# Performance work log

Measured on AMD Instinct MI355X. Metric: run time of the kernel, lower is better.

## Reference

```python
import jax, jax.numpy as jnp
import numpy as np

K = 499  # kernel_size


def setup_inputs() -> dict:
    key = jax.random.key(0)
    k1, k2 = jax.random.split(key)
    B, F, T = 32, 64, 8000
    # nonnegative spectrogram input, shape (B, 1, F, T)
    x = jax.random.uniform(k1, (B, 1, F, T), dtype=jnp.float32)
    a = 0.90 + 0.099 * jax.random.uniform(k2, (F,), dtype=jnp.float32)
    w = jnp.ones((F,), dtype=jnp.float32)
    return {"x": x, "a": a, "w": w}


def _build_kernel(a, w, dtype):
    # powers[f, k] = a_f ** k, k = 0..K-2
    F = a.shape[0]
    powers = a[:, None] ** jnp.arange(K - 1, dtype=dtype)  # (F, K-1)
    C = 1.0 / powers.sum(axis=1)                            # (F,)
    neg = (-C * w)[:, None] * powers                        # (F, K-1)
    # pre-flip kernel = [1, neg_0, ..., neg_{K-2}]; flipped -> [neg_{K-2}, ..., neg_0, 1]
    kern = jnp.concatenate([neg[:, ::-1], jnp.ones((F, 1), dtype)], axis=1)  # (F, K)
    return kern[:, None, :]  # (F, 1, K) OIH, groups = F


def reference(x, a, w):
    dtype = x.dtype
    kern = _build_kernel(a.astype(dtype), w.astype(dtype), dtype)
    xs = x[:, 0]  # (B, F, T)
    # replicate (edge) pad on the left by K-1 along time
    xp = jnp.pad(xs, ((0, 0), (0, 0), (K - 1, 0)), mode="edge")
    y = jax.lax.conv_general_dilated(
        xp, kern,
        window_strides=(1,), padding="VALID",
        dimension_numbers=("NCH", "OIH", "NCH"),
        feature_group_count=xs.shape[1],
    )  # (B, F, T)
    return jnp.abs(y)[:, None]  # (B, 1, F, T)
```

## Files before the change

### kernel.cpp

```cpp
#include <hip/hip_runtime.h>
#include <math.h>


constexpr int T     = 8000;
constexpr int F     = 64;
constexpr int B     = 32;
constexpr int KM1   = 498;
constexpr int CHUNK = 512;
constexpr int CPR   = (T + CHUNK - 1) / CHUNK;

#define DPP_F(x, ctrl, rm) \
  __builtin_bit_cast(float, __builtin_amdgcn_update_dpp(0, __builtin_bit_cast(int, (x)), (ctrl), (rm), 0xf, false))

__device__ __forceinline__ double dpow(double b, int e) {
    double r = 1.0, p = b;
    while (e) { if (e & 1) r *= p; p *= p; e >>= 1; }
    return r;
}

__device__ __forceinline__ float powi(float base, int e) {
    float r = 1.0f, p = base;
    #pragma unroll
    for (int b = 0; b < 9; ++b) { r = (e & (1 << b)) ? r * p : r; p *= p; }
    return r;
}

__global__ __launch_bounds__(256) void willmore_scan_kernel(
    const float* __restrict__ x, const float* __restrict__ a,
    const float* __restrict__ w, float* __restrict__ out)
{
    const int wid   = blockIdx.x * 4 + (threadIdx.x >> 6);
    const int lane  = threadIdx.x & 63;
    const int row   = wid >> 4;
    const int chunk = wid & (CPR - 1);
    const int f     = row % F;

    const float* xr   = x   + (size_t)row * T;
    float*       orow = out + (size_t)row * T;

    const double ad     = (double)a[f];
    const double a498d  = dpow(ad, KM1);
    const double sumgeo = (1.0 - a498d) / (1.0 - ad);
    const double r_d    = dpow(ad, 8);
    const float  af     = (float)ad;
    const float  na498  = (float)(-a498d);
    const float  g      = (float)(1.0 / sumgeo) * w[f];
    const float  r1     = (float)r_d;
    const float  r2     = (float)(r_d * r_d);
    const float  r4     = (float)dpow(r_d, 4);
    const float  r8     = (float)dpow(r_d, 8);
    const float  inv_r  = (float)(1.0 / r_d);
    const float  alane  = powi(af, 8 * lane);
    const float  wA     = powi(af, 8 * ((lane & 15) + 1));
    const float  wB     = powi(af, 8 * ((lane & 31) + 1));

    const int t0   = chunk * CHUNK;
    const int tb_u = t0 + 8 * lane;
    const int tb   = min(tb_u, T - 8);

    const float4 m0 = *(const float4*)(xr + tb);
    const float4 m1 = *(const float4*)(xr + tb + 4);

    float ws8[8];
    float lv[8];
    const int lg = tb - KM1;
    if (chunk > 0) {
        const int wb = t0 - CHUNK + 8 * lane;
        const float4 w0 = *(const float4*)(xr + wb);
        const float4 w1 = *(const float4*)(xr + wb + 4);
        ws8[0]=w0.x; ws8[1]=w0.y; ws8[2]=w0.z; ws8[3]=w0.w;
        ws8[4]=w1.x; ws8[5]=w1.y; ws8[6]=w1.z; ws8[7]=w1.w;
        const float2 p0 = *(const float2*)(xr + lg);
        const float2 p1 = *(const float2*)(xr + lg + 2);
        const float2 p2 = *(const float2*)(xr + lg + 4);
        const float2 p3 = *(const float2*)(xr + lg + 6);
        lv[0]=p0.x; lv[1]=p0.y; lv[2]=p1.x; lv[3]=p1.y;
        lv[4]=p2.x; lv[5]=p2.y; lv[6]=p3.x; lv[7]=p3.y;
    } else {
        #pragma unroll
        for (int i = 0; i < 8; ++i) lv[i] = xr[max(lg + i, 0)];
    }

    float S;
    if (chunk == 0) {
        S = m0.x;
        S = xr[0] * (float)sumgeo;
    } else {
        #pragma unroll
        for (int i = 0; i < 8; ++i) { if (8 * lane + i < 14) ws8[i] = 0.0f; }
        float h = ws8[0];
        #pragma unroll
        for (int i = 1; i < 8; ++i) h = fmaf(h, af, ws8[i]);
        float contrib = powi(af, 504 - 8 * lane) * h;
        #pragma unroll
        for (int s = 1; s < 64; s <<= 1) contrib += __shfl_xor(contrib, s, 64);
        S = contrib;
    }

    const float xv[8] = {m0.x, m0.y, m0.z, m0.w, m1.x, m1.y, m1.z, m1.w};
    float u[8];
    #pragma unroll
    for (int i = 0; i < 8; ++i) u[i] = fmaf(na498, lv[i], xv[i]);

    float q = u[0];
    #pragma unroll
    for (int i = 1; i < 8; ++i) q = fmaf(q, af, u[i]);

    float G = q;
    G = fmaf(r1, DPP_F(G, 0x111, 0xf), G);
    G = fmaf(r2, DPP_F(G, 0x112, 0xf), G);
    G = fmaf(r4, DPP_F(G, 0x114, 0xf), G);
    G = fmaf(r8, DPP_F(G, 0x118, 0xf), G);
    G = fmaf(wA, DPP_F(G, 0x142, 0xa), G);
    G = fmaf(wB, DPP_F(G, 0x143, 0xc), G);

    const float E = (G - q) * inv_r;

    float s = fmaf(alane, S, E);
    float y[8];
    #pragma unroll
    for (int i = 0; i < 8; ++i) {
        y[i] = fabsf(fmaf(-g, s, xv[i]));
        s = fmaf(af, s, u[i]);
    }

    if (tb_u <= T - 8) {
        *(float4*)(orow + tb)     = make_float4(y[0], y[1], y[2], y[3]);
        *(float4*)(orow + tb + 4) = make_float4(y[4], y[5], y[6], y[7]);
    }
}

extern "C" void kernel_launch(void* const* d_in, const int* in_sizes, int n_in,
                              void* d_out, int out_size, void* d_ws, size_t ws_size,
                              hipStream_t stream) {
    const float* x = (const float*)d_in[0];
    const float* a = (const float*)d_in[1];
    const float* w = (const float*)d_in[2];
    float* out = (float*)d_out;

    const int blocks = B * F * CPR / 4;
    hipLaunchKernelGGL(willmore_scan_kernel, dim3(blocks), dim3(256), 0, stream,
                       x, a, w, out);
}
```

Baseline: 116.6 us.

## Stage each row in LDS with one 1024-thread block per row

Launches one 1024-thread block per (batch, band) row and stages the whole row in shared memory. Each wave then reads its previous-chunk window and lagged samples from LDS instead of issuing extra global loads. This removes the redundant global reads (roughly 2x traffic) of overlapping windows. The cost is a block-wide barrier, fewer resident blocks because of the large block size and 32KB of LDS, and unaligned scalar LDS reads for the lagged values.

```diff
diff --git a/kernel.cpp b/kernel.cpp
--- a/kernel.cpp
+++ b/kernel.cpp
@@ -7,7 +7,7 @@
 constexpr int B     = 32;
 constexpr int KM1   = 498;
 constexpr int CHUNK = 512;
-constexpr int CPR   = (T + CHUNK - 1) / CHUNK;
+constexpr int CPR   = 16;
 
 #define DPP_F(x, ctrl, rm) \
   __builtin_bit_cast(float, __builtin_amdgcn_update_dpp(0, __builtin_bit_cast(int, (x)), (ctrl), (rm), 0xf, false))
@@ -25,18 +25,26 @@
     return r;
 }
 
-__global__ __launch_bounds__(256) void willmore_scan_kernel(
+__global__ __launch_bounds__(1024, 1) void willmore_scan_kernel(
     const float* __restrict__ x, const float* __restrict__ a,
     const float* __restrict__ w, float* __restrict__ out)
 {
-    const int wid   = blockIdx.x * 4 + (threadIdx.x >> 6);
+    __shared__ float lx[CPR * CHUNK];
+
+    const int chunk = threadIdx.x >> 6;
     const int lane  = threadIdx.x & 63;
-    const int row   = wid >> 4;
-    const int chunk = wid & (CPR - 1);
-    const int f     = row % F;
+    const int row   = blockIdx.x;
+    const int f     = row & (F - 1);
 
     const float* xr   = x   + (size_t)row * T;
     float*       orow = out + (size_t)row * T;
+
+    const int t0   = chunk * CHUNK;
+    const int tb_u = t0 + 8 * lane;
+    const int tb   = min(tb_u, T - 8);
+
+    const float4 m0 = *(const float4*)(xr + tb);
+    const float4 m1 = *(const float4*)(xr + tb + 4);
 
     const double ad     = (double)a[f];
     const double a498d  = dpow(ad, KM1);
@@ -54,38 +62,18 @@
     const float  wA     = powi(af, 8 * ((lane & 15) + 1));
     const float  wB     = powi(af, 8 * ((lane & 31) + 1));
 
-    const int t0   = chunk * CHUNK;
-    const int tb_u = t0 + 8 * lane;
-    const int tb   = min(tb_u, T - 8);
-
-    const float4 m0 = *(const float4*)(xr + tb);
-    const float4 m1 = *(const float4*)(xr + tb + 4);
-
-    float ws8[8];
-    float lv[8];
-    const int lg = tb - KM1;
-    if (chunk > 0) {
-        const int wb = t0 - CHUNK + 8 * lane;
-        const float4 w0 = *(const float4*)(xr + wb);
-        const float4 w1 = *(const float4*)(xr + wb + 4);
-        ws8[0]=w0.x; ws8[1]=w0.y; ws8[2]=w0.z; ws8[3]=w0.w;
-        ws8[4]=w1.x; ws8[5]=w1.y; ws8[6]=w1.z; ws8[7]=w1.w;
-        const float2 p0 = *(const float2*)(xr + lg);
-        const float2 p1 = *(const float2*)(xr + lg + 2);
-        const float2 p2 = *(const float2*)(xr + lg + 4);
-        const float2 p3 = *(const float2*)(xr + lg + 6);
-        lv[0]=p0.x; lv[1]=p0.y; lv[2]=p1.x; lv[3]=p1.y;
-        lv[4]=p2.x; lv[5]=p2.y; lv[6]=p3.x; lv[7]=p3.y;
-    } else {
-        #pragma unroll
-        for (int i = 0; i < 8; ++i) lv[i] = xr[max(lg + i, 0)];
-    }
+    *(float4*)(&lx[tb])     = m0;
+    *(float4*)(&lx[tb + 4]) = m1;
+    __syncthreads();
 
     float S;
     if (chunk == 0) {
-        S = m0.x;
-        S = xr[0] * (float)sumgeo;
+        S = lx[0] * (float)sumgeo;
     } else {
+        const int wb = t0 - CHUNK + 8 * lane;
+        const float4 w0 = *(const float4*)(&lx[wb]);
+        const float4 w1 = *(const float4*)(&lx[wb + 4]);
+        float ws8[8] = {w0.x, w0.y, w0.z, w0.w, w1.x, w1.y, w1.z, w1.w};
         #pragma unroll
         for (int i = 0; i < 8; ++i) { if (8 * lane + i < 14) ws8[i] = 0.0f; }
         float h = ws8[0];
@@ -96,6 +84,11 @@
         for (int s = 1; s < 64; s <<= 1) contrib += __shfl_xor(contrib, s, 64);
         S = contrib;
     }
+
+    const int lg = tb - KM1;
+    float lv[8];
+    #pragma unroll
+    for (int i = 0; i < 8; ++i) lv[i] = lx[max(lg + i, 0)];
 
     const float xv[8] = {m0.x, m0.y, m0.z, m0.w, m1.x, m1.y, m1.z, m1.w};
     float u[8];
@@ -138,7 +131,6 @@
     const float* w = (const float*)d_in[2];
     float* out = (float*)d_out;
 
-    const int blocks = B * F * CPR / 4;
-    hipLaunchKernelGGL(willmore_scan_kernel, dim3(blocks), dim3(256), 0, stream,
+    hipLaunchKernelGGL(willmore_scan_kernel, dim3(B * F), dim3(1024), 0, stream,
                        x, a, w, out);
 }
```

After: 114.2 us. -2.0%, faster.
